# Kernel optimization log

Measured on AMD Instinct MI355X. Metric: run time of the kernel, lower is better.

## Reference

```python
import jax, jax.numpy as jnp
import numpy as np
import math

DIM = 2048
N_HEADS = 16
HEAD_DIM = DIM // N_HEADS
BSZ = 1
SEQ = 2048


def setup_inputs() -> dict:
    key = jax.random.key(0)
    ks = jax.random.split(key, 6)
    x = jax.random.normal(ks[0], (BSZ, SEQ, DIM), dtype=jnp.float32)
    # additive ALiBi-style mask on scores [bsz, H, S_q, S_kv]
    mask = jax.random.normal(ks[1], (BSZ, N_HEADS, SEQ, SEQ), dtype=jnp.float32)
    scale = 1.0 / math.sqrt(DIM)
    wq = jax.random.normal(ks[2], (DIM, DIM), dtype=jnp.float32) * scale
    wk = jax.random.normal(ks[3], (DIM, DIM), dtype=jnp.float32) * scale
    wv = jax.random.normal(ks[4], (DIM, DIM), dtype=jnp.float32) * scale
    wo = jax.random.normal(ks[5], (DIM, DIM), dtype=jnp.float32) * scale
    return {"x": x, "mask": mask, "start_pos": 0, "wq": wq, "wk": wk, "wv": wv, "wo": wo}


def reference(x, mask, start_pos, wq, wk, wv, wo):
    bsz, seqlen, _ = x.shape
    # projections (nn.Linear applies x @ W.T)
    q = (x @ wq.T).reshape(bsz, seqlen, N_HEADS, HEAD_DIM)
    k = (x @ wk.T).reshape(bsz, seqlen, N_HEADS, HEAD_DIM)
    v = (x @ wv.T).reshape(bsz, seqlen, N_HEADS, HEAD_DIM)
    # start_pos = 0 prefill: KV = current keys/values (cache slice [:seqlen])
    # scores: [b, h, q, k]
    scores = jnp.einsum("bqhd,bkhd->bhqk", q, k) / math.sqrt(HEAD_DIM)
    scores = scores + mask
    probs = jax.nn.softmax(scores.astype(jnp.float32), axis=-1).astype(q.dtype)
    out = jnp.einsum("bhqk,bkhd->bqhd", probs, v).reshape(bsz, seqlen, -1)
    return out @ wo.T
```

## Files before the change

kernel.cpp:

```cpp
#include <hip/hip_runtime.h>
#include <stdint.h>

#define SEQ 2048
#define DIM 2048
#define NH 16
#define HD 128

typedef __attribute__((ext_vector_type(8))) short short8;
typedef __attribute__((ext_vector_type(4))) float f32x4;

#define MFMA(a, b, c) __builtin_amdgcn_mfma_f32_16x16x32_bf16((a), (b), (c), 0, 0, 0)

#define GL2LDS(gp, lp)                                                              \
    __builtin_amdgcn_global_load_lds(                                               \
        (const __attribute__((address_space(1))) void*)(gp),                        \
        (__attribute__((address_space(3))) void*)(lp), 16, 0, 0)

__device__ __forceinline__ unsigned short f2bf(float f) {
    unsigned u = __builtin_bit_cast(unsigned, f);
    u += 0x7FFFu + ((u >> 16) & 1u);
    return (unsigned short)(u >> 16);
}

__device__ __forceinline__ short8 lds_ld8(const unsigned short* p) {
    return *(const short8*)p;
}

__global__ void cvt_all(const float* __restrict__ x, const float* __restrict__ wq,
                        const float* __restrict__ wk, const float* __restrict__ wv,
                        const float* __restrict__ wo, unsigned short* __restrict__ xb,
                        unsigned short* __restrict__ wqb, unsigned short* __restrict__ wkb,
                        unsigned short* __restrict__ wvb, unsigned short* __restrict__ wob) {
    int sel = blockIdx.x >> 11;
    int lb = blockIdx.x & 2047;
    const float* src = sel == 0 ? x : sel == 1 ? wq : sel == 2 ? wk : sel == 3 ? wv : wo;
    unsigned short* dst = sel == 0 ? xb : sel == 1 ? wqb : sel == 2 ? wkb : sel == 3 ? wvb : wob;
    size_t i = ((size_t)lb * 256 + threadIdx.x) * 8;
    const f32x4* p = (const f32x4*)(src + i);
    f32x4 a = p[0], b = p[1];
    short8 r;
    r[0] = (short)f2bf(a[0]); r[1] = (short)f2bf(a[1]);
    r[2] = (short)f2bf(a[2]); r[3] = (short)f2bf(a[3]);
    r[4] = (short)f2bf(b[0]); r[5] = (short)f2bf(b[1]);
    r[6] = (short)f2bf(b[2]); r[7] = (short)f2bf(b[3]);
    *(short8*)(dst + i) = r;
}

__global__ __launch_bounds__(256, 3) void gemm_qkv(
    const unsigned short* __restrict__ xb, const unsigned short* __restrict__ wqb,
    const unsigned short* __restrict__ wkb, const unsigned short* __restrict__ wvb,
    unsigned short* __restrict__ qo, unsigned short* __restrict__ ko,
    unsigned short* __restrict__ vto) {
    __shared__ unsigned short lds[17408];
    unsigned short* Alds = lds;
    unsigned short* Blds = lds + 8192;

    const int tid = threadIdx.x;
    const int bid = blockIdx.x;
    const int mb = bid & 15;
    const int nb = bid >> 4;
    const int part = nb >> 4;
    const int nloc = (nb & 15) << 7;
    const unsigned short* __restrict__ B = part == 0 ? wqb : (part == 1 ? wkb : wvb);
    const int m0 = mb << 7;

    const int w = tid >> 6, l = tid & 63;
    const int wr = (w >> 1) * 64, wc = (w & 1) * 64;
    const int lr = l & 15, lk = l >> 4;

    f32x4 z = {0.f, 0.f, 0.f, 0.f};
    f32x4 acc[4][4];
#pragma unroll
    for (int i = 0; i < 4; i++)
#pragma unroll
        for (int j = 0; j < 4; j++) acc[i][j] = z;

    const int srow = tid >> 3;
    const int schunk = tid & 7;

    for (int kt = 0; kt < DIM; kt += 64) {
        __syncthreads();
#pragma unroll
        for (int i = 0; i < 4; i++) {
            int row = i * 32 + srow;
            int gc = (schunk ^ (row & 7)) * 8;
            GL2LDS(xb + (size_t)(m0 + row) * DIM + kt + gc, Alds + i * 2048 + tid * 8);
            GL2LDS(B + (size_t)(nloc + row) * DIM + kt + gc, Blds + i * 2048 + tid * 8);
        }
        __syncthreads();
#pragma unroll
        for (int ks = 0; ks < 2; ks++) {
            short8 af[4], bf[4];
#pragma unroll
            for (int mf = 0; mf < 4; mf++) {
                int ra = wr + mf * 16 + lr;
                af[mf] = lds_ld8(&Alds[ra * 64 + (((ks * 4 + lk) ^ (ra & 7)) * 8)]);
            }
#pragma unroll
            for (int nf = 0; nf < 4; nf++) {
                int rb = wc + nf * 16 + lr;
                bf[nf] = lds_ld8(&Blds[rb * 64 + (((ks * 4 + lk) ^ (rb & 7)) * 8)]);
            }
#pragma unroll
            for (int mf = 0; mf < 4; mf++)
#pragma unroll
                for (int nf = 0; nf < 4; nf++) acc[mf][nf] = MFMA(af[mf], bf[nf], acc[mf][nf]);
        }
    }

    if (part < 2) {
        unsigned short* dst = part == 0 ? qo : ko;
#pragma unroll
        for (int mf = 0; mf < 4; mf++)
#pragma unroll
            for (int nf = 0; nf < 4; nf++)
#pragma unroll
                for (int r = 0; r < 4; r++) {
                    int row = m0 + wr + mf * 16 + lk * 4 + r;
                    int col = nloc + wc + nf * 16 + lr;
                    dst[(size_t)row * DIM + col] = f2bf(acc[mf][nf][r]);
                }
    } else {
        const int head = nb & 15;
        __syncthreads();
#pragma unroll
        for (int mf = 0; mf < 4; mf++)
#pragma unroll
            for (int nf = 0; nf < 4; nf++)
#pragma unroll
                for (int r = 0; r < 4; r++) {
                    int d = wc + nf * 16 + lr;
                    int s = wr + mf * 16 + lk * 4 + r;
                    lds[d * 136 + s] = f2bf(acc[mf][nf][r]);
                }
        __syncthreads();
#pragma unroll
        for (int i = 0; i < 8; i++) {
            int d = (tid >> 4) + i * 16;
            int c = tid & 15;
            short8 v = *(const short8*)&lds[d * 136 + c * 8];
            *(short8*)(vto + (size_t)(head * 128 + d) * SEQ + m0 + c * 8) = v;
        }
    }
}

__global__ __launch_bounds__(256, 2) void attn_kernel(
    const unsigned short* __restrict__ qg, const unsigned short* __restrict__ kg,
    const unsigned short* __restrict__ vtg, const float* __restrict__ mask,
    unsigned short* __restrict__ ao) {
    __shared__ unsigned short Klds[64 * 136];
    __shared__ unsigned short Vlds[128 * 72];
    __shared__ unsigned short Plds[4][16 * 72];

    const int bid = blockIdx.x;
    const int h = bid >> 5;
    const int q0 = (bid & 31) << 6;
    const int tid = threadIdx.x;
    const int w = tid >> 6, l = tid & 63;
    const int lr = l & 15, lk = l >> 4;

    const float sc = 0.08838834764831845f * 1.4426950408889634f;
    const float l2e = 1.4426950408889634f;

    short8 qf[4];
    {
        const unsigned short* qp = qg + (size_t)(q0 + w * 16 + lr) * DIM + h * 128;
#pragma unroll
        for (int ks = 0; ks < 4; ks++) qf[ks] = *(const short8*)(qp + ks * 32 + lk * 8);
    }

    f32x4 z = {0.f, 0.f, 0.f, 0.f};
    f32x4 oacc[8];
#pragma unroll
    for (int i = 0; i < 8; i++) oacc[i] = z;
    float m_r[4] = {-3.0e38f, -3.0e38f, -3.0e38f, -3.0e38f};
    float l_r[4] = {0.f, 0.f, 0.f, 0.f};

    for (int kv0 = 0; kv0 < SEQ; kv0 += 64) {
        __syncthreads();
#pragma unroll
        for (int i = 0; i < 4; i++) {
            int r = i * 16 + (tid >> 4), c = tid & 15;
            *(short8*)&Klds[r * 136 + c * 8] =
                *(const short8*)(kg + (size_t)(kv0 + r) * DIM + h * 128 + c * 8);
        }
#pragma unroll
        for (int i = 0; i < 4; i++) {
            int d = i * 32 + (tid >> 3), c = tid & 7;
            *(short8*)&Vlds[d * 72 + c * 8] =
                *(const short8*)(vtg + (size_t)(h * 128 + d) * SEQ + kv0 + c * 8);
        }
        __syncthreads();

        f32x4 sacc[4];
#pragma unroll
        for (int kvf = 0; kvf < 4; kvf++) sacc[kvf] = z;
#pragma unroll
        for (int ks = 0; ks < 4; ks++)
#pragma unroll
            for (int kvf = 0; kvf < 4; kvf++) {
                short8 kf = lds_ld8(&Klds[(kvf * 16 + lr) * 136 + ks * 32 + lk * 8]);
                sacc[kvf] = MFMA(qf[ks], kf, sacc[kvf]);
            }

        const float* mrow = mask + ((size_t)h * SEQ + (q0 + w * 16 + lk * 4)) * SEQ + kv0 + lr;
        float mv[4][4];
#pragma unroll
        for (int r = 0; r < 4; r++)
#pragma unroll
            for (int kvf = 0; kvf < 4; kvf++) mv[r][kvf] = mrow[(size_t)r * SEQ + kvf * 16];

        float sv[4][4];
#pragma unroll
        for (int kvf = 0; kvf < 4; kvf++)
#pragma unroll
            for (int r = 0; r < 4; r++) sv[kvf][r] = sacc[kvf][r] * sc + mv[r][kvf] * l2e;

        float fr[4];
#pragma unroll
        for (int r = 0; r < 4; r++) {
            float mx = fmaxf(fmaxf(sv[0][r], sv[1][r]), fmaxf(sv[2][r], sv[3][r]));
            mx = fmaxf(mx, __shfl_xor(mx, 1));
            mx = fmaxf(mx, __shfl_xor(mx, 2));
            mx = fmaxf(mx, __shfl_xor(mx, 4));
            mx = fmaxf(mx, __shfl_xor(mx, 8));
            float mnew = fmaxf(m_r[r], mx);
            fr[r] = exp2f(m_r[r] - mnew);
            m_r[r] = mnew;
        }
#pragma unroll
        for (int r = 0; r < 4; r++) {
            float ps = 0.f;
#pragma unroll
            for (int kvf = 0; kvf < 4; kvf++) {
                float p = exp2f(sv[kvf][r] - m_r[r]);
                ps += p;
                Plds[w][(lk * 4 + r) * 72 + kvf * 16 + lr] = f2bf(p);
            }
            l_r[r] = l_r[r] * fr[r] + ps;
        }
#pragma unroll
        for (int dn = 0; dn < 8; dn++)
#pragma unroll
            for (int r = 0; r < 4; r++) oacc[dn][r] *= fr[r];

#pragma unroll
        for (int ksl = 0; ksl < 2; ksl++) {
            short8 pa = lds_ld8(&Plds[w][lr * 72 + ksl * 32 + lk * 8]);
#pragma unroll
            for (int dn = 0; dn < 8; dn++) {
                short8 vb = lds_ld8(&Vlds[(dn * 16 + lr) * 72 + ksl * 32 + lk * 8]);
                oacc[dn] = MFMA(pa, vb, oacc[dn]);
            }
        }
    }

#pragma unroll
    for (int r = 0; r < 4; r++) {
        float s = l_r[r];
        s += __shfl_xor(s, 1);
        s += __shfl_xor(s, 2);
        s += __shfl_xor(s, 4);
        s += __shfl_xor(s, 8);
        l_r[r] = 1.0f / s;
    }
    const int orow = q0 + w * 16 + lk * 4;
#pragma unroll
    for (int dn = 0; dn < 8; dn++)
#pragma unroll
        for (int r = 0; r < 4; r++)
            ao[(size_t)(orow + r) * DIM + h * 128 + dn * 16 + lr] = f2bf(oacc[dn][r] * l_r[r]);
}

__global__ __launch_bounds__(256, 3) void gemm_o(const unsigned short* __restrict__ ao,
                                                 const unsigned short* __restrict__ wob,
                                                 float* __restrict__ out) {
    __shared__ unsigned short lds[8192 + 4096];
    unsigned short* Alds = lds;
    unsigned short* Blds = lds + 8192;

    const int tid = threadIdx.x;
    const int bid = blockIdx.x;
    const int mb = bid & 15;
    const int nb = bid >> 4;
    const int m0 = mb << 7, n0 = nb << 6;

    const int w = tid >> 6, l = tid & 63;
    const int wr = (w >> 1) * 64, wc = (w & 1) * 32;
    const int lr = l & 15, lk = l >> 4;

    f32x4 z = {0.f, 0.f, 0.f, 0.f};
    f32x4 acc[4][2];
#pragma unroll
    for (int i = 0; i < 4; i++) {
        acc[i][0] = z;
        acc[i][1] = z;
    }

    const int srow = tid >> 3;
    const int schunk = tid & 7;

    for (int kt = 0; kt < DIM; kt += 64) {
        __syncthreads();
#pragma unroll
        for (int i = 0; i < 4; i++) {
            int row = i * 32 + srow;
            int gc = (schunk ^ (row & 7)) * 8;
            GL2LDS(ao + (size_t)(m0 + row) * DIM + kt + gc, Alds + i * 2048 + tid * 8);
        }
#pragma unroll
        for (int i = 0; i < 2; i++) {
            int row = i * 32 + srow;
            int gc = (schunk ^ (row & 7)) * 8;
            GL2LDS(wob + (size_t)(n0 + row) * DIM + kt + gc, Blds + i * 2048 + tid * 8);
        }
        __syncthreads();
#pragma unroll
        for (int ks = 0; ks < 2; ks++) {
            short8 af[4], bf[2];
#pragma unroll
            for (int mf = 0; mf < 4; mf++) {
                int ra = wr + mf * 16 + lr;
                af[mf] = lds_ld8(&Alds[ra * 64 + (((ks * 4 + lk) ^ (ra & 7)) * 8)]);
            }
#pragma unroll
            for (int nf = 0; nf < 2; nf++) {
                int rb = wc + nf * 16 + lr;
                bf[nf] = lds_ld8(&Blds[rb * 64 + (((ks * 4 + lk) ^ (rb & 7)) * 8)]);
            }
#pragma unroll
            for (int mf = 0; mf < 4; mf++)
#pragma unroll
                for (int nf = 0; nf < 2; nf++) acc[mf][nf] = MFMA(af[mf], bf[nf], acc[mf][nf]);
        }
    }

#pragma unroll
    for (int mf = 0; mf < 4; mf++)
#pragma unroll
        for (int nf = 0; nf < 2; nf++)
#pragma unroll
            for (int r = 0; r < 4; r++) {
                int row = m0 + wr + mf * 16 + lk * 4 + r;
                int col = n0 + wc + nf * 16 + lr;
                out[(size_t)row * DIM + col] = acc[mf][nf][r];
            }
}

extern "C" void kernel_launch(void* const* d_in, const int* in_sizes, int n_in, void* d_out,
                              int out_size, void* d_ws, size_t ws_size, hipStream_t stream) {
    const float* x = (const float*)d_in[0];
    const float* mask = (const float*)d_in[1];
    const float* wq = (const float*)d_in[3];
    const float* wk = (const float*)d_in[4];
    const float* wv = (const float*)d_in[5];
    const float* wo = (const float*)d_in[6];
    float* out = (float*)d_out;

    const size_t NE = (size_t)SEQ * DIM;
    const size_t NEEDED = 8 * NE * sizeof(unsigned short);
    if (ws_size < NEEDED) {
        return;
    }
    unsigned short* xb = (unsigned short*)d_ws;
    unsigned short* wqb = xb + NE;
    unsigned short* wkb = wqb + NE;
    unsigned short* wvb = wkb + NE;
    unsigned short* wob = wvb + NE;
    unsigned short* qo = wob + NE;
    unsigned short* ko = qo + NE;
    unsigned short* vto = ko + NE;
    unsigned short* ao = wqb;

    cvt_all<<<5 * 2048, 256, 0, stream>>>(x, wq, wk, wv, wo, xb, wqb, wkb, wvb, wob);
    gemm_qkv<<<768, 256, 0, stream>>>(xb, wqb, wkb, wvb, qo, ko, vto);
    attn_kernel<<<512, 256, 0, stream>>>(qo, ko, vto, mask, ao);
    gemm_o<<<512, 256, 0, stream>>>(ao, wob, out);
}
```

Before: 544.2 us.

## Prefetch next K/V tile and mask block into registers during attention compute

The attention loop now issues global loads for the next KV tile's K, V and mask values into registers right after the LDS store barrier, so they overlap with the current tile's QK MFMAs, softmax and PV MFMAs. Previously each iteration loaded K/V synchronously before compute and fetched the mask after the QK product, which exposed global memory latency. The trade-off is higher register pressure (extra K/V short8 and 16 mask floats), which could reduce occupancy.

```diff
diff --git a/kernel.cpp b/kernel.cpp
--- a/kernel.cpp
+++ b/kernel.cpp
@@ -169,6 +169,26 @@
         for (int ks = 0; ks < 4; ks++) qf[ks] = *(const short8*)(qp + ks * 32 + lk * 8);
     }
 
+    const int krow = tid >> 4, kcol = tid & 15;
+    const int vrow = tid >> 3, vcol = tid & 7;
+    const unsigned short* kbase = kg + (size_t)h * 128;
+    const unsigned short* vbase = vtg + (size_t)h * 128 * SEQ;
+    const float* mbase = mask + ((size_t)h * SEQ + (q0 + w * 16 + lk * 4)) * SEQ + lr;
+
+    short8 kreg[4], vreg[4];
+    float mv[4][4], mvn[4][4];
+
+#pragma unroll
+    for (int i = 0; i < 4; i++)
+        kreg[i] = *(const short8*)(kbase + (size_t)(i * 16 + krow) * DIM + kcol * 8);
+#pragma unroll
+    for (int i = 0; i < 4; i++)
+        vreg[i] = *(const short8*)(vbase + (size_t)(i * 32 + vrow) * SEQ + vcol * 8);
+#pragma unroll
+    for (int r = 0; r < 4; r++)
+#pragma unroll
+        for (int kvf = 0; kvf < 4; kvf++) mv[r][kvf] = mbase[(size_t)r * SEQ + kvf * 16];
+
     f32x4 z = {0.f, 0.f, 0.f, 0.f};
     f32x4 oacc[8];
 #pragma unroll
@@ -179,18 +199,27 @@
     for (int kv0 = 0; kv0 < SEQ; kv0 += 64) {
         __syncthreads();
 #pragma unroll
-        for (int i = 0; i < 4; i++) {
-            int r = i * 16 + (tid >> 4), c = tid & 15;
-            *(short8*)&Klds[r * 136 + c * 8] =
-                *(const short8*)(kg + (size_t)(kv0 + r) * DIM + h * 128 + c * 8);
-        }
-#pragma unroll
-        for (int i = 0; i < 4; i++) {
-            int d = i * 32 + (tid >> 3), c = tid & 7;
-            *(short8*)&Vlds[d * 72 + c * 8] =
-                *(const short8*)(vtg + (size_t)(h * 128 + d) * SEQ + kv0 + c * 8);
-        }
-        __syncthreads();
+        for (int i = 0; i < 4; i++)
+            *(short8*)&Klds[(i * 16 + krow) * 136 + kcol * 8] = kreg[i];
+#pragma unroll
+        for (int i = 0; i < 4; i++)
+            *(short8*)&Vlds[(i * 32 + vrow) * 72 + vcol * 8] = vreg[i];
+        __syncthreads();
+
+        if (kv0 + 64 < SEQ) {
+            int nx = kv0 + 64;
+#pragma unroll
+            for (int i = 0; i < 4; i++)
+                kreg[i] = *(const short8*)(kbase + (size_t)(nx + i * 16 + krow) * DIM + kcol * 8);
+#pragma unroll
+            for (int i = 0; i < 4; i++)
+                vreg[i] = *(const short8*)(vbase + (size_t)(i * 32 + vrow) * SEQ + nx + vcol * 8);
+#pragma unroll
+            for (int r = 0; r < 4; r++)
+#pragma unroll
+                for (int kvf = 0; kvf < 4; kvf++)
+                    mvn[r][kvf] = mbase[(size_t)r * SEQ + nx + kvf * 16];
+        }
 
         f32x4 sacc[4];
 #pragma unroll
@@ -202,13 +231,6 @@
                 short8 kf = lds_ld8(&Klds[(kvf * 16 + lr) * 136 + ks * 32 + lk * 8]);
                 sacc[kvf] = MFMA(qf[ks], kf, sacc[kvf]);
             }
-
-        const float* mrow = mask + ((size_t)h * SEQ + (q0 + w * 16 + lk * 4)) * SEQ + kv0 + lr;
-        float mv[4][4];
-#pragma unroll
-        for (int r = 0; r < 4; r++)
-#pragma unroll
-            for (int kvf = 0; kvf < 4; kvf++) mv[r][kvf] = mrow[(size_t)r * SEQ + kvf * 16];
 
         float sv[4][4];
 #pragma unroll
@@ -253,6 +275,11 @@
                 oacc[dn] = MFMA(pa, vb, oacc[dn]);
             }
         }
+
+#pragma unroll
+        for (int r = 0; r < 4; r++)
+#pragma unroll
+            for (int kvf = 0; kvf < 4; kvf++) mv[r][kvf] = mvn[r][kvf];
     }
 
 #pragma unroll
```

Result: slower. 560.1 us (+2.9%).
